# Optimization experiments

Hardware: AMD Instinct MI355X
Metric: run time of the kernel (lower is better)

The kernel has to match this reference:

```python
import jax, jax.numpy as jnp
import numpy as np

OUT_F, IN_F = 4096, 4096
NNZ = 838860
TOKENS = (8, 2048)


def setup_inputs() -> dict:
    key = jax.random.key(0)
    k1, k2, k3, k4, k5 = jax.random.split(key, 5)
    inp = {
        "input": jax.random.normal(k1, (*TOKENS, IN_F), dtype=jnp.float32),
        "dense_weights": jax.random.normal(k2, (OUT_F, IN_F), dtype=jnp.float32) * 0.02,
        "dense_bias": jax.random.normal(k3, (OUT_F,), dtype=jnp.float32) * 0.02,
        "sparse_weights": jax.random.normal(k4, (NNZ,), dtype=jnp.float32) * 0.02,
        "nz_idx": jnp.sort(jax.random.randint(k5, (NNZ,), 0, OUT_F * IN_F, dtype=jnp.int32)),
    }
    return inp


def reference(input, dense_weights, dense_bias, sparse_weights, nz_idx):
    # csr_add: scatter sparse delta into dense weight (CSR expressed as sorted flat indices)
    out_f, in_f = dense_weights.shape
    rows = nz_idx // in_f
    cols = nz_idx % in_f
    weights = dense_weights.at[rows, cols].add(sparse_weights)  # [out_f, in_f]
    # F.linear: x @ W.T + b
    return jnp.einsum('bsi,oi->bso', input, weights) + dense_bias
```

## Files before the change

kernel.cpp:

```cpp
#include <hip/hip_runtime.h>

typedef __bf16 bf16x8 __attribute__((ext_vector_type(8)));
typedef float  f32x4  __attribute__((ext_vector_type(4)));

#define IN_F  4096
#define OUT_F 4096
#define TM 128
#define TN 128
#define BK 32

__device__ inline unsigned int pk_bf16(float a, float b) {
  unsigned int ua = __float_as_uint(a);
  unsigned int ub = __float_as_uint(b);
  ua = (ua + 0x7FFFu + ((ua >> 16) & 1u)) >> 16;
  ub = (ub + 0x7FFFu + ((ub >> 16) & 1u)) >> 16;
  return ua | (ub << 16);
}

__global__ void copy_f32x4(const float4* __restrict__ src, float4* __restrict__ dst, int n4) {
  int i = blockIdx.x * 256 + threadIdx.x;
  if (i < n4) dst[i] = src[i];
}

__global__ void scatter_add_k(float* __restrict__ w, const int* __restrict__ idx,
                              const float* __restrict__ v, int nnz) {
  int i = blockIdx.x * 256 + threadIdx.x;
  if (i < nnz) atomicAdd(w + idx[i], v[i]);
}

__global__ void cvt_f32_bf16_x8(const float4* __restrict__ src, uint4* __restrict__ dst, int n8) {
  int i = blockIdx.x * 256 + threadIdx.x;
  if (i >= n8) return;
  float4 a = src[2 * i];
  float4 b = src[2 * i + 1];
  uint4 o;
  o.x = pk_bf16(a.x, a.y);
  o.y = pk_bf16(a.z, a.w);
  o.z = pk_bf16(b.x, b.y);
  o.w = pk_bf16(b.z, b.w);
  dst[i] = o;
}

__global__ __launch_bounds__(256, 2) void gemm_bt_bias(
    const unsigned short* __restrict__ Xb,
    const unsigned short* __restrict__ Wb,
    const float* __restrict__ bias,
    float* __restrict__ out,
    int M, int N, int K)
{
  __shared__ unsigned short lds_a[TM * BK];
  __shared__ unsigned short lds_b[TN * BK];

  const int t    = threadIdx.x;
  const int wave = t >> 6;
  const int lane = t & 63;
  const int quad = lane >> 4;
  const int l16  = lane & 15;

  const int tile_n = blockIdx.x * TN;
  const int tile_m = blockIdx.y * TM;

  const int wm = (wave >> 1) * 64;
  const int wn = (wave & 1) * 64;

  f32x4 acc[4][4] = {};

  const unsigned short* Ag = Xb + (size_t)tile_m * K;
  const unsigned short* Bg = Wb + (size_t)tile_n * K;

  const int c0 = t, c1 = 256 + t;
  const int row0 = c0 >> 2, row1 = c1 >> 2;
  const int kc0 = (((c0 & 3) ^ ((row0 >> 1) & 3)) * 8);
  const int kc1 = (((c1 & 3) ^ ((row1 >> 1) & 3)) * 8);

  for (int kb = 0; kb < K; kb += BK) {
    __syncthreads();
    __builtin_amdgcn_global_load_lds(
        (const __attribute__((address_space(1))) unsigned int*)(Ag + (size_t)row0 * K + kb + kc0),
        (__attribute__((address_space(3))) unsigned int*)(lds_a + c0 * 8), 16, 0, 0);
    __builtin_amdgcn_global_load_lds(
        (const __attribute__((address_space(1))) unsigned int*)(Ag + (size_t)row1 * K + kb + kc1),
        (__attribute__((address_space(3))) unsigned int*)(lds_a + c1 * 8), 16, 0, 0);
    __builtin_amdgcn_global_load_lds(
        (const __attribute__((address_space(1))) unsigned int*)(Bg + (size_t)row0 * K + kb + kc0),
        (__attribute__((address_space(3))) unsigned int*)(lds_b + c0 * 8), 16, 0, 0);
    __builtin_amdgcn_global_load_lds(
        (const __attribute__((address_space(1))) unsigned int*)(Bg + (size_t)row1 * K + kb + kc1),
        (__attribute__((address_space(3))) unsigned int*)(lds_b + c1 * 8), 16, 0, 0);
    __syncthreads();

    bf16x8 af[4], bfr[4];
#pragma unroll
    for (int i = 0; i < 4; ++i) {
      const int ra = wm + i * 16 + l16;
      const int rb = wn + i * 16 + l16;
      const int ca = (quad ^ ((ra >> 1) & 3)) * 8;
      const int cb = (quad ^ ((rb >> 1) & 3)) * 8;
      af[i]  = *(const bf16x8*)&lds_a[ra * BK + ca];
      bfr[i] = *(const bf16x8*)&lds_b[rb * BK + cb];
    }
#pragma unroll
    for (int i = 0; i < 4; ++i)
#pragma unroll
      for (int j = 0; j < 4; ++j)
        acc[i][j] = __builtin_amdgcn_mfma_f32_16x16x32_bf16(af[i], bfr[j], acc[i][j], 0, 0, 0);
  }

#pragma unroll
  for (int j = 0; j < 4; ++j) {
    const int n = tile_n + wn + j * 16 + l16;
    const float bv = bias[n];
#pragma unroll
    for (int i = 0; i < 4; ++i) {
      const int m0 = tile_m + wm + i * 16 + quad * 4;
#pragma unroll
      for (int r = 0; r < 4; ++r) {
        out[(size_t)(m0 + r) * N + n] = acc[i][j][r] + bv;
      }
    }
  }
}

extern "C" void kernel_launch(void* const* d_in, const int* in_sizes, int n_in,
                              void* d_out, int out_size, void* d_ws, size_t ws_size,
                              hipStream_t stream) {
  const float* x    = (const float*)d_in[0];
  const float* dw   = (const float*)d_in[1];
  const float* bias = (const float*)d_in[2];
  const float* sv   = (const float*)d_in[3];
  const int*   idx  = (const int*)d_in[4];
  float* out = (float*)d_out;

  const int K = IN_F, N = OUT_F;
  const int M   = in_sizes[0] / K;
  const int nnz = in_sizes[3];
  const int WN  = N * K;

  float*          ws_w  = (float*)d_ws;
  unsigned short* ws_wb = (unsigned short*)((char*)d_ws + (size_t)WN * 4);
  unsigned short* ws_xb = (unsigned short*)((char*)d_ws + (size_t)WN * 4 + (size_t)WN * 2);

  copy_f32x4<<<WN / 4 / 256, 256, 0, stream>>>((const float4*)dw, (float4*)ws_w, WN / 4);
  scatter_add_k<<<(nnz + 255) / 256, 256, 0, stream>>>(ws_w, idx, sv, nnz);
  cvt_f32_bf16_x8<<<WN / 8 / 256, 256, 0, stream>>>((const float4*)ws_w, (uint4*)ws_wb, WN / 8);
  const int xn = in_sizes[0];
  cvt_f32_bf16_x8<<<xn / 8 / 256, 256, 0, stream>>>((const float4*)x, (uint4*)ws_xb, xn / 8);
  dim3 grid(N / TN, M / TM);
  gemm_bt_bias<<<grid, 256, 0, stream>>>(ws_xb, ws_wb, bias, out, M, N, K);
}
```

Measured before the change: 1.109 ms.

## Rewrite GEMM as 256x256 multi-buffered pipeline and fuse sparse update into bf16 weights

```diff
diff --git a/kernel.cpp b/kernel.cpp
--- a/kernel.cpp
+++ b/kernel.cpp
@@ -5,9 +5,11 @@
 
 #define IN_F  4096
 #define OUT_F 4096
-#define TM 128
-#define TN 128
+#define BM 256
+#define BN 256
 #define BK 32
+#define NBUF 4
+#define TILE_ELEMS (BM * BK)
 
 __device__ inline unsigned int pk_bf16(float a, float b) {
   unsigned int ua = __float_as_uint(a);
@@ -16,16 +18,9 @@
   ub = (ub + 0x7FFFu + ((ub >> 16) & 1u)) >> 16;
   return ua | (ub << 16);
 }
-
-__global__ void copy_f32x4(const float4* __restrict__ src, float4* __restrict__ dst, int n4) {
-  int i = blockIdx.x * 256 + threadIdx.x;
-  if (i < n4) dst[i] = src[i];
-}
-
-__global__ void scatter_add_k(float* __restrict__ w, const int* __restrict__ idx,
-                              const float* __restrict__ v, int nnz) {
-  int i = blockIdx.x * 256 + threadIdx.x;
-  if (i < nnz) atomicAdd(w + idx[i], v[i]);
+__device__ inline unsigned short bf16_1(float a) {
+  unsigned int u = __float_as_uint(a);
+  return (unsigned short)((u + 0x7FFFu + ((u >> 16) & 1u)) >> 16);
 }
 
 __global__ void cvt_f32_bf16_x8(const float4* __restrict__ src, uint4* __restrict__ dst, int n8) {
@@ -41,84 +36,135 @@
   dst[i] = o;
 }
 
-__global__ __launch_bounds__(256, 2) void gemm_bt_bias(
+__global__ void sparse_fix_k(const float* __restrict__ dw, const int* __restrict__ idx,
+                             const float* __restrict__ sv, unsigned short* __restrict__ wb,
+                             int nnz) {
+  int i = blockIdx.x * 256 + threadIdx.x;
+  if (i >= nnz) return;
+  int id = idx[i];
+  if (i > 0 && idx[i - 1] == id) return;
+  float s = sv[i];
+  int j = i + 1;
+  while (j < nnz && idx[j] == id) { s += sv[j]; ++j; }
+  wb[id] = bf16_1(dw[id] + s);
+}
+
+__global__ __launch_bounds__(512, 2) void gemm256(
     const unsigned short* __restrict__ Xb,
     const unsigned short* __restrict__ Wb,
     const float* __restrict__ bias,
     float* __restrict__ out,
     int M, int N, int K)
 {
-  __shared__ unsigned short lds_a[TM * BK];
-  __shared__ unsigned short lds_b[TN * BK];
+  __shared__ __align__(16) unsigned short lA[NBUF * TILE_ELEMS];
+  __shared__ __align__(16) unsigned short lB[NBUF * TILE_ELEMS];
 
   const int t    = threadIdx.x;
-  const int wave = t >> 6;
+  const int w    = t >> 6;
   const int lane = t & 63;
   const int quad = lane >> 4;
   const int l16  = lane & 15;
+  const int wr   = w >> 2;
+  const int wc   = w & 3;
 
-  const int tile_n = blockIdx.x * TN;
-  const int tile_m = blockIdx.y * TM;
+  const int nwg = gridDim.x;
+  const int cpx = nwg >> 3;
+  const int sid = (blockIdx.x & 7) * cpx + (blockIdx.x >> 3);
+  const int gn  = N / BN;
+  const int tile_n = (sid % gn) * BN;
+  const int tile_m = (sid / gn) * BM;
 
-  const int wm = (wave >> 1) * 64;
-  const int wn = (wave & 1) * 64;
+  const int c0 = t, c1 = 512 + t;
+  const int r0 = c0 >> 2, r1 = c1 >> 2;
+  const int s0 = ((c0 & 3) ^ ((r0 >> 1) & 3)) * 8;
+  const int s1 = ((c1 & 3) ^ ((r1 >> 1) & 3)) * 8;
+  const unsigned short* aS0 = Xb + (size_t)(tile_m + r0) * K + s0;
+  const unsigned short* aS1 = Xb + (size_t)(tile_m + r1) * K + s1;
+  const unsigned short* bS0 = Wb + (size_t)(tile_n + r0) * K + s0;
+  const unsigned short* bS1 = Wb + (size_t)(tile_n + r1) * K + s1;
 
-  f32x4 acc[4][4] = {};
+#define GLD(src, dst) __builtin_amdgcn_global_load_lds( \
+      (const __attribute__((address_space(1))) unsigned int*)(src), \
+      (__attribute__((address_space(3))) unsigned int*)(dst), 16, 0, 0)
+#define STAGE_A(tt) do { const int _b = ((tt) & 3) * TILE_ELEMS; const int _kb = (tt) * BK; \
+      GLD(aS0 + _kb, lA + _b + c0 * 8); GLD(aS1 + _kb, lA + _b + c1 * 8); } while (0)
+#define STAGE_B(tt) do { const int _b = ((tt) & 3) * TILE_ELEMS; const int _kb = (tt) * BK; \
+      GLD(bS0 + _kb, lB + _b + c0 * 8); GLD(bS1 + _kb, lB + _b + c1 * 8); } while (0)
 
-  const unsigned short* Ag = Xb + (size_t)tile_m * K;
-  const unsigned short* Bg = Wb + (size_t)tile_n * K;
+  int offA[8], offB[4];
+#pragma unroll
+  for (int mi = 0; mi < 8; ++mi) {
+    const int ra = wr * 128 + mi * 16 + l16;
+    offA[mi] = ra * BK + (quad ^ ((ra >> 1) & 3)) * 8;
+  }
+#pragma unroll
+  for (int ni = 0; ni < 4; ++ni) {
+    const int rb = wc * 64 + ni * 16 + l16;
+    offB[ni] = rb * BK + (quad ^ ((rb >> 1) & 3)) * 8;
+  }
 
-  const int c0 = t, c1 = 256 + t;
-  const int row0 = c0 >> 2, row1 = c1 >> 2;
-  const int kc0 = (((c0 & 3) ^ ((row0 >> 1) & 3)) * 8);
-  const int kc1 = (((c1 & 3) ^ ((row1 >> 1) & 3)) * 8);
+  f32x4 acc[8][4] = {};
+  const int nt = K / BK;
 
-  for (int kb = 0; kb < K; kb += BK) {
-    __syncthreads();
-    __builtin_amdgcn_global_load_lds(
-        (const __attribute__((address_space(1))) unsigned int*)(Ag + (size_t)row0 * K + kb + kc0),
-        (__attribute__((address_space(3))) unsigned int*)(lds_a + c0 * 8), 16, 0, 0);
-    __builtin_amdgcn_global_load_lds(
-        (const __attribute__((address_space(1))) unsigned int*)(Ag + (size_t)row1 * K + kb + kc1),
-        (__attribute__((address_space(3))) unsigned int*)(lds_a + c1 * 8), 16, 0, 0);
-    __builtin_amdgcn_global_load_lds(
-        (const __attribute__((address_space(1))) unsigned int*)(Bg + (size_t)row0 * K + kb + kc0),
-        (__attribute__((address_space(3))) unsigned int*)(lds_b + c0 * 8), 16, 0, 0);
-    __builtin_amdgcn_global_load_lds(
-        (const __attribute__((address_space(1))) unsigned int*)(Bg + (size_t)row1 * K + kb + kc1),
-        (__attribute__((address_space(3))) unsigned int*)(lds_b + c1 * 8), 16, 0, 0);
-    __syncthreads();
+  STAGE_A(0); STAGE_B(0);
+  STAGE_A(1); STAGE_B(1);
+  STAGE_A(2); STAGE_B(2);
+  asm volatile("s_waitcnt vmcnt(8)" ::: "memory");
+  __builtin_amdgcn_s_barrier();
 
-    bf16x8 af[4], bfr[4];
+  for (int tt = 0; tt < nt; ++tt) {
+    const unsigned short* bufA = lA + (tt & 3) * TILE_ELEMS;
+    const unsigned short* bufB = lB + (tt & 3) * TILE_ELEMS;
+
+    bf16x8 af0[4], bfr[4];
 #pragma unroll
-    for (int i = 0; i < 4; ++i) {
-      const int ra = wm + i * 16 + l16;
-      const int rb = wn + i * 16 + l16;
-      const int ca = (quad ^ ((ra >> 1) & 3)) * 8;
-      const int cb = (quad ^ ((rb >> 1) & 3)) * 8;
-      af[i]  = *(const bf16x8*)&lds_a[ra * BK + ca];
-      bfr[i] = *(const bf16x8*)&lds_b[rb * BK + cb];
-    }
+    for (int mi = 0; mi < 4; ++mi) af0[mi] = *(const bf16x8*)&bufA[offA[mi]];
 #pragma unroll
-    for (int i = 0; i < 4; ++i)
+    for (int ni = 0; ni < 4; ++ni) bfr[ni] = *(const bf16x8*)&bufB[offB[ni]];
+    if (tt + 3 < nt) STAGE_A(tt + 3);
+    __builtin_amdgcn_s_barrier();
+    __builtin_amdgcn_s_setprio(1);
 #pragma unroll
-      for (int j = 0; j < 4; ++j)
-        acc[i][j] = __builtin_amdgcn_mfma_f32_16x16x32_bf16(af[i], bfr[j], acc[i][j], 0, 0, 0);
+    for (int mi = 0; mi < 4; ++mi)
+#pragma unroll
+      for (int ni = 0; ni < 4; ++ni)
+        acc[mi][ni] = __builtin_amdgcn_mfma_f32_16x16x32_bf16(af0[mi], bfr[ni], acc[mi][ni], 0, 0, 0);
+    __builtin_amdgcn_s_setprio(0);
+    __builtin_amdgcn_s_barrier();
+
+    bf16x8 af1[4];
+#pragma unroll
+    for (int mi = 0; mi < 4; ++mi) af1[mi] = *(const bf16x8*)&bufA[offA[4 + mi]];
+    if (tt + 3 < nt) STAGE_B(tt + 3);
+    if (tt < nt - 3)       asm volatile("s_waitcnt vmcnt(8)" ::: "memory");
+    else if (tt == nt - 3) asm volatile("s_waitcnt vmcnt(4)" ::: "memory");
+    else if (tt == nt - 2) asm volatile("s_waitcnt vmcnt(0)" ::: "memory");
+    __builtin_amdgcn_s_barrier();
+    __builtin_amdgcn_s_setprio(1);
+#pragma unroll
+    for (int mi = 0; mi < 4; ++mi)
+#pragma unroll
+      for (int ni = 0; ni < 4; ++ni)
+        acc[4 + mi][ni] = __builtin_amdgcn_mfma_f32_16x16x32_bf16(af1[mi], bfr[ni], acc[4 + mi][ni], 0, 0, 0);
+    __builtin_amdgcn_s_setprio(0);
+    __builtin_amdgcn_s_barrier();
   }
 
 #pragma unroll
-  for (int j = 0; j < 4; ++j) {
-    const int n = tile_n + wn + j * 16 + l16;
+  for (int ni = 0; ni < 4; ++ni) {
+    const int n = tile_n + wc * 64 + ni * 16 + l16;
     const float bv = bias[n];
 #pragma unroll
-    for (int i = 0; i < 4; ++i) {
-      const int m0 = tile_m + wm + i * 16 + quad * 4;
+    for (int mi = 0; mi < 8; ++mi) {
+      const int m0 = tile_m + wr * 128 + mi * 16 + quad * 4;
 #pragma unroll
-      for (int r = 0; r < 4; ++r) {
-        out[(size_t)(m0 + r) * N + n] = acc[i][j][r] + bv;
-      }
+      for (int r = 0; r < 4; ++r)
+        out[(size_t)(m0 + r) * N + n] = acc[mi][ni][r] + bv;
     }
   }
+#undef GLD
+#undef STAGE_A
+#undef STAGE_B
 }
 
 extern "C" void kernel_launch(void* const* d_in, const int* in_sizes, int n_in,
@@ -136,15 +182,13 @@
   const int nnz = in_sizes[3];
   const int WN  = N * K;
 
-  float*          ws_w  = (float*)d_ws;
-  unsigned short* ws_wb = (unsigned short*)((char*)d_ws + (size_t)WN * 4);
-  unsigned short* ws_xb = (unsigned short*)((char*)d_ws + (size_t)WN * 4 + (size_t)WN * 2);
+  unsigned short* ws_xb = (unsigned short*)d_ws;
+  unsigned short* ws_wb = (unsigned short*)((char*)d_ws + (size_t)in_sizes[0] * 2);
 
-  copy_f32x4<<<WN / 4 / 256, 256, 0, stream>>>((const float4*)dw, (float4*)ws_w, WN / 4);
-  scatter_add_k<<<(nnz + 255) / 256, 256, 0, stream>>>(ws_w, idx, sv, nnz);
-  cvt_f32_bf16_x8<<<WN / 8 / 256, 256, 0, stream>>>((const float4*)ws_w, (uint4*)ws_wb, WN / 8);
+  cvt_f32_bf16_x8<<<WN / 8 / 256, 256, 0, stream>>>((const float4*)dw, (uint4*)ws_wb, WN / 8);
+  sparse_fix_k<<<(nnz + 255) / 256, 256, 0, stream>>>(dw, idx, sv, ws_wb, nnz);
   const int xn = in_sizes[0];
   cvt_f32_bf16_x8<<<xn / 8 / 256, 256, 0, stream>>>((const float4*)x, (uint4*)ws_xb, xn / 8);
-  dim3 grid(N / TN, M / TM);
-  gemm_bt_bias<<<grid, 256, 0, stream>>>(ws_xb, ws_wb, bias, out, M, N, K);
+  const int nblocks = (M / BM) * (N / BN);
+  gemm256<<<nblocks, 512, 0, stream>>>(ws_xb, ws_wb, bias, out, M, N, K);
 }
```

Result: faster. 1.067 ms (-3.8%).
